# Kernel tuning notes

Measured on AMD Instinct MI355X. Metric: run time of the kernel, lower is better.

The kernel has to match this reference:

```python
import jax, jax.numpy as jnp
import numpy as np

N = 50000
LEAKY_SLOPE = 0.2


def gat_layer(x, src, dst, W, a_src, a_dst, bias, concat):
    """PyG-style GATConv (eval mode, self-loops already in src/dst).
    x: [N, Fin]; W: [Fin, H*C]; a_src, a_dst: [H, C]; bias: [H*C] or [C].
    """
    H, C = a_src.shape
    h = (x @ W).reshape(-1, H, C)                      # [N, H, C]
    alpha_src = jnp.einsum('nhc,hc->nh', h, a_src)      # [N, H]
    alpha_dst = jnp.einsum('nhc,hc->nh', h, a_dst)      # [N, H]
    e = jax.nn.leaky_relu(alpha_src[src] + alpha_dst[dst], LEAKY_SLOPE)  # [E, H]
    # scatter-softmax over incoming edges of each destination node
    m = jax.lax.stop_gradient(jax.ops.segment_max(e, dst, num_segments=N))
    e = jnp.exp(e - m[dst])
    denom = jax.ops.segment_sum(e, dst, num_segments=N)  # [N, H]
    alpha = e / (denom[dst] + 1e-16)                     # [E, H]
    msg = h[src] * alpha[:, :, None]                     # [E, H, C]
    out = jax.ops.segment_sum(msg, dst, num_segments=N)  # [N, H, C]
    out = out.reshape(-1, H * C) if concat else out.mean(axis=1)
    return out + bias


def setup_inputs() -> dict:
    key = jax.random.key(0)
    ks = jax.random.split(key, 10)
    Fin, Hd, Hh = 256, 64, 4
    E = 1600000
    x = jax.random.normal(ks[0], (N, Fin), dtype=jnp.float32)
    edge_index = jax.random.randint(ks[1], (2, E), 0, N, dtype=jnp.int64)
    s = 1.0 / np.sqrt(Fin)
    W1 = jax.random.normal(ks[2], (Fin, Hh * Hd), dtype=jnp.float32) * s
    att_src1 = jax.random.normal(ks[3], (Hh, Hd), dtype=jnp.float32) * (1.0 / np.sqrt(Hd))
    att_dst1 = jax.random.normal(ks[4], (Hh, Hd), dtype=jnp.float32) * (1.0 / np.sqrt(Hd))
    b1 = jnp.zeros((Hh * Hd,), dtype=jnp.float32)
    W2 = jax.random.normal(ks[5], (Hh * Hd, Hd), dtype=jnp.float32) * (1.0 / np.sqrt(Hh * Hd))
    att_src2 = jax.random.normal(ks[6], (1, Hd), dtype=jnp.float32) * (1.0 / np.sqrt(Hd))
    att_dst2 = jax.random.normal(ks[7], (1, Hd), dtype=jnp.float32) * (1.0 / np.sqrt(Hd))
    b2 = jnp.zeros((Hd,), dtype=jnp.float32)
    return {"x": x, "edge_index": edge_index, "W1": W1, "att_src1": att_src1,
            "att_dst1": att_dst1, "b1": b1, "W2": W2, "att_src2": att_src2,
            "att_dst2": att_dst2, "b2": b2}


def reference(x, edge_index, W1, att_src1, att_dst1, b1, W2, att_src2, att_dst2, b2):
    # PyG GATConv adds self-loops by default
    loop = jnp.arange(N, dtype=edge_index.dtype)
    src = jnp.concatenate([edge_index[0], loop])
    dst = jnp.concatenate([edge_index[1], loop])
    h = gat_layer(x, src, dst, W1, att_src1, att_dst1, b1, concat=True)
    h = jax.nn.elu(h)            # dropout is identity in eval mode
    out = gat_layer(h, src, dst, W2, att_src2, att_dst2, b2, concat=False)
    return out
```

## Files before the change

kernel.cpp:

```cpp
#include <hip/hip_runtime.h>


typedef __attribute__((ext_vector_type(8))) short short8;
typedef __attribute__((ext_vector_type(4))) float floatx4;
typedef __attribute__((ext_vector_type(2))) float fx2;

#define FIN 256
#define H1 4
#define CH 64
#define CAP 16384

__device__ __forceinline__ float bf2f(ushort u) {
    union { unsigned int i; float f; } v; v.i = ((unsigned int)u) << 16; return v.f;
}
__device__ __forceinline__ ushort f2bf(float f) {
    union { float f; unsigned int i; } v; v.f = f;
    unsigned int r = v.i + 0x7fffu + ((v.i >> 16) & 1u);
    return (ushort)(r >> 16);
}
__device__ __forceinline__ float load_in(const void* p, int i, int f) {
    return f ? ((const float*)p)[i] : bf2f(((const ushort*)p)[i]);
}
__device__ __forceinline__ int load_idx(const void* p, long long i, int f64) {
    return f64 ? (int)((const long long*)p)[i] : ((const int*)p)[i];
}

__device__ __forceinline__ float edge_p(float s) {
    s = fmaxf(s, 0.2f * s);
    return __expf(s);
}

__device__ __forceinline__ void accum16(fx2* acc, uint4 v0, uint4 v1,
                                        float p, float& l) {
    l += p;
    fx2 pv = {p, p};
    unsigned w[8] = {v0.x, v0.y, v0.z, v0.w, v1.x, v1.y, v1.z, v1.w};
#pragma unroll
    for (int u = 0; u < 8; ++u) {
        union { unsigned i; float fl; } lo, hi;
        lo.i = w[u] << 16; hi.i = w[u] & 0xffff0000u;
        fx2 c = {lo.fl, hi.fl};
        acc[u] += pv * c;
    }
}

__device__ __forceinline__ void accum8(fx2* acc, uint4 v, float p, float& l) {
    l += p;
    fx2 pv = {p, p};
    unsigned w[4] = {v.x, v.y, v.z, v.w};
#pragma unroll
    for (int u = 0; u < 4; ++u) {
        union { unsigned i; float fl; } lo, hi;
        lo.i = w[u] << 16; hi.i = w[u] & 0xffff0000u;
        fx2 c = {lo.fl, hi.fl};
        acc[u] += pv * c;
    }
}

__global__ __launch_bounds__(256) void probe_kernel(const ushort* __restrict__ x,
                                                    const int* __restrict__ ei,
                                                    int* __restrict__ flags,
                                                    int* __restrict__ bcnt) {
    __shared__ int s_nan, s_odd;
    int t = threadIdx.x;
    bcnt[t] = 0;
    if (t == 0) { s_nan = 0; s_odd = 0; }
    __syncthreads();
    int nanc = 0, oddc = 0;
    for (int i = t; i < 16384; i += 256) {
        ushort u = x[i];
        if (((u >> 7) & 0xFF) == 0xFF) nanc++;
    }
    for (int i = t; i < 2048; i += 256)
        if (ei[2 * i + 1] != 0) oddc++;
    if (nanc) atomicAdd(&s_nan, nanc);
    if (oddc) atomicAdd(&s_odd, oddc);
    __syncthreads();
    if (t == 0) {
        flags[0] = (s_nan >= 2) ? 1 : 0;
        flags[1] = (s_odd == 0) ? 1 : 0;
    }
}

__global__ __launch_bounds__(256) void prep_bucket_kernel(
        const void* __restrict__ x, const void* __restrict__ W1,
        const void* __restrict__ W2, ushort* __restrict__ xb,
        ushort* __restrict__ Wt1, ushort* __restrict__ Wt2,
        const void* __restrict__ ei, int* __restrict__ bcnt,
        unsigned int* __restrict__ buckets,
        int E, int Etot, int Nn, const int* __restrict__ flags,
        int PB_conv, int PB_tr_end) {
    __shared__ int lcnt[256], lbase[256], lcur[256];
    int bid = blockIdx.x, t = threadIdx.x;
    int f = flags[0];
    if (bid < PB_conv) {
        int i0 = bid * 2048 + t * 8;
        if (f) {
            float4 v0 = ((const float4*)x)[i0 / 4];
            float4 v1 = ((const float4*)x)[i0 / 4 + 1];
            ushort4 o0, o1;
            o0.x = f2bf(v0.x); o0.y = f2bf(v0.y); o0.z = f2bf(v0.z); o0.w = f2bf(v0.w);
            o1.x = f2bf(v1.x); o1.y = f2bf(v1.y); o1.z = f2bf(v1.z); o1.w = f2bf(v1.w);
            *(ushort4*)(xb + i0) = o0;
            *(ushort4*)(xb + i0 + 4) = o1;
        } else {
            *(uint4*)(xb + i0) = ((const uint4*)x)[i0 / 8];
        }
        return;
    }
    if (bid < PB_tr_end) {
        int j = (bid - PB_conv) * 256 + t;
        if (j < FIN * FIN) {
            int n = j / FIN, k = j % FIN;
            Wt1[j] = f2bf(load_in(W1, k * FIN + n, f));
        } else {
            int jj = j - FIN * FIN;
            int n = jj / FIN, k = jj % FIN;
            Wt2[jj] = f2bf(load_in(W2, k * CH + n, f));
        }
        return;
    }
    lcnt[t] = 0; lcur[t] = 0;
    __syncthreads();
    int f64 = flags[1];
    int base = (bid - PB_tr_end) * 4096 + t;
    unsigned int val[16]; int bk[16]; bool ok[16];
#pragma unroll
    for (int j = 0; j < 16; ++j) {
        int e = base + j * 256;
        ok[j] = e < Etot;
        bk[j] = 0; val[j] = 0;
        if (ok[j]) {
            int s, d;
            if (e < E) {
                s = load_idx(ei, e, f64);
                d = load_idx(ei, (long long)E + e, f64);
            } else {
                s = d = e - E;
            }
            s = min(max(s, 0), Nn - 1);
            d = min(max(d, 0), Nn - 1);
            bk[j] = d >> 8;
            val[j] = ((unsigned int)s << 8) | (unsigned int)(d & 255);
            atomicAdd(&lcnt[bk[j]], 1);
        }
    }
    __syncthreads();
    if (lcnt[t] > 0) lbase[t] = atomicAdd(&bcnt[t], lcnt[t]);
    __syncthreads();
#pragma unroll
    for (int j = 0; j < 16; ++j) {
        if (ok[j]) {
            int p = lbase[bk[j]] + atomicAdd(&lcur[bk[j]], 1);
            if (p < CAP) buckets[(size_t)bk[j] * CAP + p] = val[j];
        }
    }
}

__device__ __forceinline__ void gemm_core(const ushort* __restrict__ A,
                                          const ushort* __restrict__ Bt,
                                          ushort* __restrict__ C,
                                          int M, int K, int Nc,
                                          const void* __restrict__ aS,
                                          const void* __restrict__ aD,
                                          float* __restrict__ alphaS,
                                          float* __restrict__ alphaD,
                                          int H, int f, int gx, int head,
                                          int planar) {
    int tid = threadIdx.x;
    int wave = tid >> 6, lane = tid & 63, quad = lane >> 4, l16 = lane & 15;
    int rbase = gx * 256 + wave * 64;
    int cbase = head * 64;
    floatx4 acc[4][4];
#pragma unroll
    for (int i = 0; i < 4; i++)
#pragma unroll
        for (int j = 0; j < 4; j++) acc[i][j] = (floatx4)0.f;

    for (int kb = 0; kb < K; kb += 32) {
        int k0 = kb + quad * 8;
        short8 a[4], b[4];
#pragma unroll
        for (int mt = 0; mt < 4; mt++) {
            int row = rbase + mt * 16 + l16;
            if (row >= M) row = M - 1;
            a[mt] = *reinterpret_cast<const short8*>(A + (size_t)row * K + k0);
        }
#pragma unroll
        for (int nt = 0; nt < 4; nt++) {
            int col = cbase + nt * 16 + l16;
            b[nt] = *reinterpret_cast<const short8*>(Bt + (size_t)col * K + k0);
        }
#pragma unroll
        for (int mt = 0; mt < 4; mt++)
#pragma unroll
            for (int nt = 0; nt < 4; nt++)
                acc[mt][nt] = __builtin_amdgcn_mfma_f32_16x16x32_bf16(
                    a[mt], b[nt], acc[mt][nt], 0, 0, 0);
    }
    float asv[4], adv[4];
#pragma unroll
    for (int nt = 0; nt < 4; nt++) {
        int col = cbase + nt * 16 + l16;
        asv[nt] = load_in(aS, col, f);
        adv[nt] = load_in(aD, col, f);
    }
#pragma unroll
    for (int mt = 0; mt < 4; mt++) {
#pragma unroll
        for (int r = 0; r < 4; r++) {
            int row = rbase + mt * 16 + quad * 4 + r;
            float ps = 0.f, pd = 0.f;
#pragma unroll
            for (int nt = 0; nt < 4; nt++) {
                float w = acc[mt][nt][r];
                ps += w * asv[nt];
                pd += w * adv[nt];
            }
#pragma unroll
            for (int off = 8; off > 0; off >>= 1) {
                ps += __shfl_xor(ps, off, 16);
                pd += __shfl_xor(pd, off, 16);
            }
            if (row < M) {
                if (l16 == 0) {
                    alphaS[row * H + head] = ps;
                    alphaD[row * H + head] = pd;
                }
#pragma unroll
                for (int nt = 0; nt < 4; nt++) {
                    int col = cbase + nt * 16 + l16;
                    size_t caddr = planar
                        ? ((size_t)(col >> 7) * M + row) * 128 + (col & 127)
                        : (size_t)row * Nc + col;
                    C[caddr] = f2bf(acc[mt][nt][r]);
                }
            }
        }
    }
}

__global__ __launch_bounds__(256) void gemm1_pass2_kernel(
        const ushort* __restrict__ A, const ushort* __restrict__ Bt,
        ushort* __restrict__ C, int M, int K, int Nc,
        const void* __restrict__ aS, const void* __restrict__ aD,
        float* __restrict__ alphaS, float* __restrict__ alphaD,
        const int* __restrict__ flags, int g1, int nbx,
        const int* __restrict__ bcnt, const unsigned int* __restrict__ buckets,
        int* __restrict__ offs, int* __restrict__ csr_src, int Nn) {
    __shared__ int part[256], sc[256], cur[256];
    int bid = blockIdx.x;
    int t = threadIdx.x;
    if (bid < g1) {
        gemm_core(A, Bt, C, M, K, Nc, aS, aD, alphaS, alphaD, 4, flags[0],
                  bid % nbx, bid / nbx, 1);
        return;
    }
    int b = bid - g1;
    part[t] = bcnt[t];
    __syncthreads();
#pragma unroll
    for (int off = 1; off < 256; off <<= 1) {
        int v = (t >= off) ? part[t - off] : 0;
        __syncthreads();
        part[t] += v;
        __syncthreads();
    }
    int basepos = (b == 0) ? 0 : part[b - 1];
    int nEdges = min(bcnt[b], CAP);
    sc[t] = 0;
    __syncthreads();
    const unsigned int* bk = buckets + (size_t)b * CAP;
    for (int i = t; i < nEdges; i += 256)
        atomicAdd(&sc[bk[i] & 255], 1);
    __syncthreads();
    int mycount = sc[t];
    __syncthreads();
#pragma unroll
    for (int off = 1; off < 256; off <<= 1) {
        int v = (t >= off) ? sc[t - off] : 0;
        __syncthreads();
        sc[t] += v;
        __syncthreads();
    }
    int excl = sc[t] - mycount;
    int gnode = b * 256 + t;
    if (gnode <= Nn) offs[gnode] = basepos + excl;
    cur[t] = excl;
    __syncthreads();
    for (int i = t; i < nEdges; i += 256) {
        unsigned int v = bk[i];
        int p = atomicAdd(&cur[v & 255], 1);
        csr_src[basepos + p] = (int)(v >> 8);
    }
}

__global__ __launch_bounds__(256) void gemm2_kernel(const ushort* __restrict__ A,
                                                    const ushort* __restrict__ Bt,
                                                    ushort* __restrict__ C,
                                                    int M, int K, int Nc,
                                                    const void* __restrict__ aS,
                                                    const void* __restrict__ aD,
                                                    float* __restrict__ alphaS,
                                                    float* __restrict__ alphaD,
                                                    const int* __restrict__ flags) {
    gemm_core(A, Bt, C, M, K, Nc, aS, aD, alphaS, alphaD, 1, flags[0],
              blockIdx.x, blockIdx.y, 0);
}

__global__ __launch_bounds__(256) void gat_node1_pass(
        const int* __restrict__ csr_src, const int* __restrict__ offs,
        const float* __restrict__ asrc, const float* __restrict__ adst,
        const ushort* __restrict__ h1p, const void* __restrict__ b1,
        ushort* __restrict__ hmidb, int Nn, const int* __restrict__ flags,
        int plane) {
    int f = flags[0];
    int wave = threadIdx.x >> 6, lane = threadIdx.x & 63;
    int n = blockIdx.x * 4 + wave;
    if (n >= Nn) return;
    int slot = lane >> 3, cg = lane & 7;
    int head = plane * 2 + (cg >> 2);
    float ad = adst[n * H1 + head];
    unsigned rowbase = (unsigned)(plane * Nn) * 128u + (unsigned)cg * 16u;
    int beg = offs[n], end = offs[n + 1];
    fx2 acc[8];
#pragma unroll
    for (int u = 0; u < 8; ++u) acc[u] = (fx2)0.f;
    float l = 0.f;

    int e = beg;
    while (e + 16 <= end) {
        int sa = csr_src[e + slot];
        int sb = csr_src[e + 8 + slot];
        float aa = asrc[sa * H1 + head];
        float ab = asrc[sb * H1 + head];
        const uint4* ra = (const uint4*)(h1p + rowbase + (unsigned)sa * 128u);
        const uint4* rb = (const uint4*)(h1p + rowbase + (unsigned)sb * 128u);
        uint4 va0 = ra[0], va1 = ra[1];
        uint4 vb0 = rb[0], vb1 = rb[1];
        float pa = edge_p(aa + ad);
        float pb = edge_p(ab + ad);
        accum16(acc, va0, va1, pa, l);
        accum16(acc, vb0, vb1, pb, l);
        e += 16;
    }
    if (e < end) {
        int ea = e + slot, eb = e + 8 + slot;
        bool oka = ea < end, okb = eb < end;
        int sa = csr_src[oka ? ea : beg];
        int sb = csr_src[okb ? eb : beg];
        float aa = asrc[sa * H1 + head];
        float ab = asrc[sb * H1 + head];
        const uint4* ra = (const uint4*)(h1p + rowbase + (unsigned)sa * 128u);
        const uint4* rb = (const uint4*)(h1p + rowbase + (unsigned)sb * 128u);
        uint4 va0 = ra[0], va1 = ra[1];
        uint4 vb0 = rb[0], vb1 = rb[1];
        float pa = edge_p(oka ? aa + ad : -1e30f);
        float pb = edge_p(okb ? ab + ad : -1e30f);
        accum16(acc, va0, va1, pa, l);
        accum16(acc, vb0, vb1, pb, l);
    }
#pragma unroll
    for (int off = 8; off <= 32; off <<= 1) {
#pragma unroll
        for (int u = 0; u < 8; ++u) {
            acc[u][0] += __shfl_xor(acc[u][0], off);
            acc[u][1] += __shfl_xor(acc[u][1], off);
        }
        l += __shfl_xor(l, off);
    }
    if (slot == 0) {
        float inv = 1.f / (l + 1e-16f);
        int cb = plane * 128 + cg * 16;
        unsigned ow[8];
#pragma unroll
        for (int u = 0; u < 8; ++u) {
            float o0 = acc[u][0] * inv + load_in(b1, cb + 2 * u, f);
            float o1 = acc[u][1] * inv + load_in(b1, cb + 2 * u + 1, f);
            o0 = o0 > 0.f ? o0 : __expf(o0) - 1.f;
            o1 = o1 > 0.f ? o1 : __expf(o1) - 1.f;
            ow[u] = (unsigned)f2bf(o0) | ((unsigned)f2bf(o1) << 16);
        }
        uint4 st0, st1;
        st0.x = ow[0]; st0.y = ow[1]; st0.z = ow[2]; st0.w = ow[3];
        st1.x = ow[4]; st1.y = ow[5]; st1.z = ow[6]; st1.w = ow[7];
        uint4* dst = (uint4*)(hmidb + (unsigned)n * 256u + (unsigned)cb);
        dst[0] = st0; dst[1] = st1;
    }
}

__global__ __launch_bounds__(256) void gat_node2(const int* __restrict__ csr_src,
                                                 const int* __restrict__ offs,
                                                 const float* __restrict__ asrc,
                                                 const float* __restrict__ adst,
                                                 const ushort* __restrict__ h2b,
                                                 const void* __restrict__ b2,
                                                 void* __restrict__ out, int Nn,
                                                 const int* __restrict__ flags) {
    int f = flags[0];
    int wave = threadIdx.x >> 6, lane = threadIdx.x & 63;
    int n = blockIdx.x * 4 + wave;
    if (n >= Nn) return;
    int slot = lane >> 3, cg = lane & 7;
    float ad = adst[n];
    unsigned rowoff = (unsigned)cg * 8u;
    int beg = offs[n], end = offs[n + 1];
    fx2 acc[4];
#pragma unroll
    for (int u = 0; u < 4; ++u) acc[u] = (fx2)0.f;
    float l = 0.f;

    int e = beg;
    while (e + 16 <= end) {
        int sa = csr_src[e + slot];
        int sb = csr_src[e + 8 + slot];
        float aa = asrc[sa];
        float ab = asrc[sb];
        uint4 va = *(const uint4*)(h2b + rowoff + (unsigned)sa * 64u);
        uint4 vb = *(const uint4*)(h2b + rowoff + (unsigned)sb * 64u);
        float pa = edge_p(aa + ad);
        float pb = edge_p(ab + ad);
        accum8(acc, va, pa, l);
        accum8(acc, vb, pb, l);
        e += 16;
    }
    if (e < end) {
        int ea = e + slot, eb = e + 8 + slot;
        bool oka = ea < end, okb = eb < end;
        int sa = csr_src[oka ? ea : beg];
        int sb = csr_src[okb ? eb : beg];
        float aa = asrc[sa];
        float ab = asrc[sb];
        uint4 va = *(const uint4*)(h2b + rowoff + (unsigned)sa * 64u);
        uint4 vb = *(const uint4*)(h2b + rowoff + (unsigned)sb * 64u);
        float pa = edge_p(oka ? aa + ad : -1e30f);
        float pb = edge_p(okb ? ab + ad : -1e30f);
        accum8(acc, va, pa, l);
        accum8(acc, vb, pb, l);
    }
#pragma unroll
    for (int off = 8; off <= 32; off <<= 1) {
#pragma unroll
        for (int u = 0; u < 4; ++u) {
            acc[u][0] += __shfl_xor(acc[u][0], off);
            acc[u][1] += __shfl_xor(acc[u][1], off);
        }
        l += __shfl_xor(l, off);
    }
    if (slot == 0) {
        float inv = 1.f / (l + 1e-16f);
        float o[8];
#pragma unroll
        for (int u = 0; u < 4; ++u) {
            o[2 * u]     = acc[u][0] * inv + load_in(b2, cg * 8 + 2 * u, f);
            o[2 * u + 1] = acc[u][1] * inv + load_in(b2, cg * 8 + 2 * u + 1, f);
        }
        if (f) {
            float* op = (float*)out + (unsigned)n * 64u + (unsigned)cg * 8u;
            float4 s0, s1;
            s0.x = o[0]; s0.y = o[1]; s0.z = o[2]; s0.w = o[3];
            s1.x = o[4]; s1.y = o[5]; s1.z = o[6]; s1.w = o[7];
            *(float4*)op = s0;
            *(float4*)(op + 4) = s1;
        } else {
            uint4 st;
            st.x = (unsigned)f2bf(o[0]) | ((unsigned)f2bf(o[1]) << 16);
            st.y = (unsigned)f2bf(o[2]) | ((unsigned)f2bf(o[3]) << 16);
            st.z = (unsigned)f2bf(o[4]) | ((unsigned)f2bf(o[5]) << 16);
            st.w = (unsigned)f2bf(o[6]) | ((unsigned)f2bf(o[7]) << 16);
            *(uint4*)((ushort*)out + (unsigned)n * 64u + (unsigned)cg * 8u) = st;
        }
    }
}

extern "C" void kernel_launch(void* const* d_in, const int* in_sizes, int n_in,
                              void* d_out, int out_size, void* d_ws, size_t ws_size,
                              hipStream_t stream) {
    const void* x   = d_in[0];
    const void* ei  = d_in[1];
    const void* W1  = d_in[2];
    const void* as1 = d_in[3];
    const void* ad1 = d_in[4];
    const void* b1  = d_in[5];
    const void* W2  = d_in[6];
    const void* as2 = d_in[7];
    const void* ad2 = d_in[8];
    const void* b2  = d_in[9];

    const int Nn = in_sizes[0] / FIN;
    const int E  = in_sizes[1] / 2;
    const int ET = E + Nn;
    const int NB = (Nn + 255) >> 8;

    char* ws = (char*)d_ws;
    size_t off = 0;
    auto alloc = [&](size_t bytes) {
        size_t o = off;
        off += (bytes + 255) & ~(size_t)255;
        return o;
    };
    ushort* xb    = (ushort*)(ws + alloc((size_t)Nn * FIN * 2));
    ushort* h1b   = (ushort*)(ws + alloc((size_t)Nn * FIN * 2));
    ushort* hmidb = (ushort*)(ws + alloc((size_t)Nn * FIN * 2));
    ushort* h2b   = (ushort*)(ws + alloc((size_t)Nn * CH * 2));
    ushort* Wt1   = (ushort*)(ws + alloc((size_t)FIN * FIN * 2));
    ushort* Wt2   = (ushort*)(ws + alloc((size_t)CH * FIN * 2));
    float* as1f   = (float*)(ws + alloc((size_t)Nn * H1 * 4));
    float* ad1f   = (float*)(ws + alloc((size_t)Nn * H1 * 4));
    float* as2f   = (float*)(ws + alloc((size_t)Nn * 4));
    float* ad2f   = (float*)(ws + alloc((size_t)Nn * 4));
    int*   offs   = (int*)(ws + alloc((size_t)(Nn + 1) * 4));
    int*   csr    = (int*)(ws + alloc((size_t)ET * 4));
    unsigned int* buckets = (unsigned int*)(ws + alloc((size_t)256 * CAP * 4));
    int*   bcnt   = (int*)(ws + alloc(256 * 4));
    int*   flags  = (int*)(ws + alloc(256));
    (void)ws_size; (void)n_in; (void)out_size;

    probe_kernel<<<1, 256, 0, stream>>>((const ushort*)x, (const int*)ei, flags, bcnt);

    int PB_conv = (Nn * FIN) / 2048;
    int PB_tr   = (FIN * FIN + CH * FIN) / 256;
    int PB_bkt  = (ET + 4095) / 4096;
    prep_bucket_kernel<<<PB_conv + PB_tr + PB_bkt, 256, 0, stream>>>(
        x, W1, W2, xb, Wt1, Wt2, ei, bcnt, buckets,
        E, ET, Nn, flags, PB_conv, PB_conv + PB_tr);

    int nbx = (Nn + 255) / 256;
    int g1 = nbx * H1;
    gemm1_pass2_kernel<<<g1 + NB, 256, 0, stream>>>(
        xb, Wt1, h1b, Nn, FIN, FIN, as1, ad1, as1f, ad1f,
        flags, g1, nbx, bcnt, buckets, offs, csr, Nn);

    gat_node1_pass<<<(Nn + 3) / 4, 256, 0, stream>>>(
        csr, offs, as1f, ad1f, h1b, b1, hmidb, Nn, flags, 0);
    gat_node1_pass<<<(Nn + 3) / 4, 256, 0, stream>>>(
        csr, offs, as1f, ad1f, h1b, b1, hmidb, Nn, flags, 1);

    gemm2_kernel<<<dim3((Nn + 255) / 256, 1), 256, 0, stream>>>(
        hmidb, Wt2, h2b, Nn, FIN, CH, as2, ad2, as2f, ad2f, flags);
    gat_node2<<<(Nn + 3) / 4, 256, 0, stream>>>(csr, offs, as2f, ad2f, h2b, b2, d_out, Nn, flags);
}
```

Baseline: 361.6 us.

## Precompute edge softmax weights and aggregate over narrow 32-column feature planes

Adds a separate kernel that computes the per-edge exponentiated attention weights and per-node inverse denominators once and writes them to workspace. The GEMMs now write features into 32-column planes, including GEMM2, which was row-major before. The aggregation is split into 8 passes for layer 1 and 2 for layer 2, each gathering 64-byte rows. The aim is to keep each plane's gather working set cache-resident and cut per-pass work. The cost is extra launches, storing and re-reading the per-edge weight arrays, and re-reading the CSR once per pass.

```diff
diff --git a/kernel.cpp b/kernel.cpp
--- a/kernel.cpp
+++ b/kernel.cpp
@@ -30,31 +30,15 @@
     return __expf(s);
 }
 
-__device__ __forceinline__ void accum16(fx2* acc, uint4 v0, uint4 v1,
-                                        float p, float& l) {
-    l += p;
+__device__ __forceinline__ void accum4(fx2& a0, fx2& a1, uint2 v, float p) {
     fx2 pv = {p, p};
-    unsigned w[8] = {v0.x, v0.y, v0.z, v0.w, v1.x, v1.y, v1.z, v1.w};
-#pragma unroll
-    for (int u = 0; u < 8; ++u) {
-        union { unsigned i; float fl; } lo, hi;
-        lo.i = w[u] << 16; hi.i = w[u] & 0xffff0000u;
-        fx2 c = {lo.fl, hi.fl};
-        acc[u] += pv * c;
-    }
-}
-
-__device__ __forceinline__ void accum8(fx2* acc, uint4 v, float p, float& l) {
-    l += p;
-    fx2 pv = {p, p};
-    unsigned w[4] = {v.x, v.y, v.z, v.w};
-#pragma unroll
-    for (int u = 0; u < 4; ++u) {
-        union { unsigned i; float fl; } lo, hi;
-        lo.i = w[u] << 16; hi.i = w[u] & 0xffff0000u;
-        fx2 c = {lo.fl, hi.fl};
-        acc[u] += pv * c;
-    }
+    union { unsigned i; float fl; } lo, hi;
+    lo.i = v.x << 16; hi.i = v.x & 0xffff0000u;
+    fx2 c0 = {lo.fl, hi.fl};
+    a0 += pv * c0;
+    lo.i = v.y << 16; hi.i = v.y & 0xffff0000u;
+    fx2 c1 = {lo.fl, hi.fl};
+    a1 += pv * c1;
 }
 
 __global__ __launch_bounds__(256) void probe_kernel(const ushort* __restrict__ x,
@@ -231,7 +215,7 @@
                 for (int nt = 0; nt < 4; nt++) {
                     int col = cbase + nt * 16 + l16;
                     size_t caddr = planar
-                        ? ((size_t)(col >> 7) * M + row) * 128 + (col & 127)
+                        ? ((size_t)(col >> 5) * M + row) * 32 + (col & 31)
                         : (size_t)row * Nc + col;
                     C[caddr] = f2bf(acc[mt][nt][r]);
                 }
@@ -305,43 +289,76 @@
                                                     float* __restrict__ alphaD,
                                                     const int* __restrict__ flags) {
     gemm_core(A, Bt, C, M, K, Nc, aS, aD, alphaS, alphaD, 1, flags[0],
-              blockIdx.x, blockIdx.y, 0);
-}
-
-__global__ __launch_bounds__(256) void gat_node1_pass(
+              blockIdx.x, blockIdx.y, 1);
+}
+
+template <int H>
+__global__ __launch_bounds__(256) void gat_edge_w(
         const int* __restrict__ csr_src, const int* __restrict__ offs,
-        const float* __restrict__ asrc, const float* __restrict__ adst,
-        const ushort* __restrict__ h1p, const void* __restrict__ b1,
+        const float* __restrict__ asf, const float* __restrict__ adf,
+        float* __restrict__ pw, float* __restrict__ linv,
+        int Nn, int ET) {
+    int wave = threadIdx.x >> 6, lane = threadIdx.x & 63;
+    int n = blockIdx.x * 4 + wave;
+    if (n >= Nn) return;
+    int beg = offs[n], end = offs[n + 1];
+    float ad[H], l[H];
+#pragma unroll
+    for (int h = 0; h < H; ++h) { ad[h] = adf[n * H + h]; l[h] = 0.f; }
+    for (int e = beg; e < end; e += 64) {
+        int pos = e + lane;
+        bool ok = pos < end;
+        int s = csr_src[ok ? pos : beg];
+        float av[H];
+        if (H == 4) {
+            float4 v = *(const float4*)(asf + s * 4);
+            av[0] = v.x; av[1 % H] = v.y; av[2 % H] = v.z; av[3 % H] = v.w;
+        } else {
+            av[0] = asf[s];
+        }
+#pragma unroll
+        for (int h = 0; h < H; ++h) {
+            float p = edge_p(ok ? av[h] + ad[h] : -1e30f);
+            l[h] += p;
+            if (ok) pw[(size_t)h * ET + pos] = p;
+        }
+    }
+#pragma unroll
+    for (int h = 0; h < H; ++h) {
+#pragma unroll
+        for (int off = 1; off <= 32; off <<= 1) l[h] += __shfl_xor(l[h], off);
+    }
+    if (lane == 0) {
+#pragma unroll
+        for (int h = 0; h < H; ++h) linv[n * H + h] = 1.f / (l[h] + 1e-16f);
+    }
+}
+
+__global__ __launch_bounds__(256) void gat_agg1(
+        const int* __restrict__ csr_src, const int* __restrict__ offs,
+        const float* __restrict__ pw, const float* __restrict__ linv,
+        const ushort* __restrict__ plane, const void* __restrict__ b1,
         ushort* __restrict__ hmidb, int Nn, const int* __restrict__ flags,
-        int plane) {
+        int q) {
     int f = flags[0];
     int wave = threadIdx.x >> 6, lane = threadIdx.x & 63;
     int n = blockIdx.x * 4 + wave;
     if (n >= Nn) return;
     int slot = lane >> 3, cg = lane & 7;
-    int head = plane * 2 + (cg >> 2);
-    float ad = adst[n * H1 + head];
-    unsigned rowbase = (unsigned)(plane * Nn) * 128u + (unsigned)cg * 16u;
     int beg = offs[n], end = offs[n + 1];
-    fx2 acc[8];
-#pragma unroll
-    for (int u = 0; u < 8; ++u) acc[u] = (fx2)0.f;
-    float l = 0.f;
+    fx2 a0 = (fx2)0.f, a1 = (fx2)0.f;
 
     int e = beg;
     while (e + 16 <= end) {
-        int sa = csr_src[e + slot];
-        int sb = csr_src[e + 8 + slot];
-        float aa = asrc[sa * H1 + head];
-        float ab = asrc[sb * H1 + head];
-        const uint4* ra = (const uint4*)(h1p + rowbase + (unsigned)sa * 128u);
-        const uint4* rb = (const uint4*)(h1p + rowbase + (unsigned)sb * 128u);
-        uint4 va0 = ra[0], va1 = ra[1];
-        uint4 vb0 = rb[0], vb1 = rb[1];
-        float pa = edge_p(aa + ad);
-        float pb = edge_p(ab + ad);
-        accum16(acc, va0, va1, pa, l);
-        accum16(acc, vb0, vb1, pb, l);
+        int pa_ = e + slot, pb_ = e + 8 + slot;
+        int sa = __builtin_nontemporal_load(csr_src + pa_);
+        int sb = __builtin_nontemporal_load(csr_src + pb_);
+        float pa = __builtin_nontemporal_load(pw + pa_);
+        float pb = __builtin_nontemporal_load(pw + pb_);
+        uint2 va = *(const uint2*)(plane + (size_t)sa * 32 + cg * 4);
+        uint2 vb = *(const uint2*)(plane + (size_t)sb * 32 + cg * 4);
+        accum4(a0, a1, va, pa);
+        accum4(a0, a1, vb, pb);
         e += 16;
     }
     if (e < end) {
@@ -349,79 +366,63 @@
         bool oka = ea < end, okb = eb < end;
         int sa = csr_src[oka ? ea : beg];
         int sb = csr_src[okb ? eb : beg];
-        float aa = asrc[sa * H1 + head];
-        float ab = asrc[sb * H1 + head];
-        const uint4* ra = (const uint4*)(h1p + rowbase + (unsigned)sa * 128u);
-        const uint4* rb = (const uint4*)(h1p + rowbase + (unsigned)sb * 128u);
-        uint4 va0 = ra[0], va1 = ra[1];
-        uint4 vb0 = rb[0], vb1 = rb[1];
-        float pa = edge_p(oka ? aa + ad : -1e30f);
-        float pb = edge_p(okb ? ab + ad : -1e30f);
-        accum16(acc, va0, va1, pa, l);
-        accum16(acc, vb0, vb1, pb, l);
+        float pa = oka ? pw[ea] : 0.f;
+        float pb = okb ? pw[eb] : 0.f;
+        uint2 va = *(const uint2*)(plane + (size_t)sa * 32 + cg * 4);
+        uint2 vb = *(const uint2*)(plane + (size_t)sb * 32 + cg * 4);
+        accum4(a0, a1, va, pa);
+        accum4(a0, a1, vb, pb);
     }
 #pragma unroll
     for (int off = 8; off <= 32; off <<= 1) {
-#pragma unroll
-        for (int u = 0; u < 8; ++u) {
-            acc[u][0] += __shfl_xor(acc[u][0], off);
-            acc[u][1] += __shfl_xor(acc[u][1], off);
-        }
-        l += __shfl_xor(l, off);
+        a0[0] += __shfl_xor(a0[0], off);
+        a0[1] += __shfl_xor(a0[1], off);
+        a1[0] += __shfl_xor(a1[0], off);
+        a1[1] += __shfl_xor(a1[1], off);
     }
     if (slot == 0) {
-        float inv = 1.f / (l + 1e-16f);
-        int cb = plane * 128 + cg * 16;
-        unsigned ow[8];
-#pragma unroll
-        for (int u = 0; u < 8; ++u) {
-            float o0 = acc[u][0] * inv + load_in(b1, cb + 2 * u, f);
-            float o1 = acc[u][1] * inv + load_in(b1, cb + 2 * u + 1, f);
-            o0 = o0 > 0.f ? o0 : __expf(o0) - 1.f;
-            o1 = o1 > 0.f ? o1 : __expf(o1) - 1.f;
-            ow[u] = (unsigned)f2bf(o0) | ((unsigned)f2bf(o1) << 16);
-        }
-        uint4 st0, st1;
-        st0.x = ow[0]; st0.y = ow[1]; st0.z = ow[2]; st0.w = ow[3];
-        st1.x = ow[4]; st1.y = ow[5]; st1.z = ow[6]; st1.w = ow[7];
-        uint4* dst = (uint4*)(hmidb + (unsigned)n * 256u + (unsigned)cb);
-        dst[0] = st0; dst[1] = st1;
-    }
-}
-
-__global__ __launch_bounds__(256) void gat_node2(const int* __restrict__ csr_src,
-                                                 const int* __restrict__ offs,
-                                                 const float* __restrict__ asrc,
-                                                 const float* __restrict__ adst,
-                                                 const ushort* __restrict__ h2b,
-                                                 const void* __restrict__ b2,
-                                                 void* __restrict__ out, int Nn,
-                                                 const int* __restrict__ flags) {
+        float inv = linv[n * H1 + (q >> 1)];
+        int cb = q * 32 + cg * 4;
+        float o0 = a0[0] * inv + load_in(b1, cb + 0, f);
+        float o1 = a0[1] * inv + load_in(b1, cb + 1, f);
+        float o2 = a1[0] * inv + load_in(b1, cb + 2, f);
+        float o3 = a1[1] * inv + load_in(b1, cb + 3, f);
+        o0 = o0 > 0.f ? o0 : __expf(o0) - 1.f;
+        o1 = o1 > 0.f ? o1 : __expf(o1) - 1.f;
+        o2 = o2 > 0.f ? o2 : __expf(o2) - 1.f;
+        o3 = o3 > 0.f ? o3 : __expf(o3) - 1.f;
+        uint2 st;
+        st.x = (unsigned)f2bf(o0) | ((unsigned)f2bf(o1) << 16);
+        st.y = (unsigned)f2bf(o2) | ((unsigned)f2bf(o3) << 16);
+        *(uint2*)(hmidb + (size_t)n * 256 + cb) = st;
+    }
+}
+
+__global__ __launch_bounds__(256) void gat_agg2(
+        const int* __restrict__ csr_src, const int* __restrict__ offs,
+        const float* __restrict__ pw, const float* __restrict__ linv,
+        const ushort* __restrict__ plane, const void* __restrict__ b2,
+        void* __restrict__ out, int Nn, const int* __restrict__ flags,
+        int q) {
     int f = flags[0];
     int wave = threadIdx.x >> 6, lane = threadIdx.x & 63;
     int n = blockIdx.x * 4 + wave;
     if (n >= Nn) return;
     int slot = lane >> 3, cg = lane & 7;
-    float ad = adst[n];
-    unsigned rowoff = (unsigned)cg * 8u;
     int beg = offs[n], end = offs[n + 1];
-    fx2 acc[4];
-#pragma unroll
-    for (int u = 0; u < 4; ++u) acc[u] = (fx2)0.f;
-    float l = 0.f;
+    fx2 a0 = (fx2)0.f, a1 = (fx2)0.f;
 
     int e = beg;
     while (e + 16 <= end) {
-        int sa = csr_src[e + slot];
-        int sb = csr_src[e + 8 + slot];
-        float aa = asrc[sa];
-        float ab = asrc[sb];
-        uint4 va = *(const uint4*)(h2b + rowoff + (unsigned)sa * 64u);
-        uint4 vb = *(const uint4*)(h2b + rowoff + (unsigned)sb * 64u);
-        float pa = edge_p(aa + ad);
-        float pb = edge_p(ab + ad);
-        accum8(acc, va, pa, l);
-        accum8(acc, vb, pb, l);
+        int pa_ = e + slot, pb_ = e + 8 + slot;
+        int sa = __builtin_nontemporal_load(csr_src + pa_);
+        int sb = __builtin_nontemporal_load(csr_src + pb_);
+        float pa = __builtin_nontemporal_load(pw + pa_);
+        float pb = __builtin_nontemporal_load(pw + pb_);
+        uint2 va = *(const uint2*)(plane + (size_t)sa * 32 + cg * 4);
+        uint2 vb = *(const uint2*)(plane + (size_t)sb * 32 + cg * 4);
+        accum4(a0, a1, va, pa);
+        accum4(a0, a1, vb, pb);
         e += 16;
     }
     if (e < end) {
@@ -429,46 +430,35 @@
         bool oka = ea < end, okb = eb < end;
         int sa = csr_src[oka ? ea : beg];
         int sb = csr_src[okb ? eb : beg];
-        float aa = asrc[sa];
-        float ab = asrc[sb];
-        uint4 va = *(const uint4*)(h2b + rowoff + (unsigned)sa * 64u);
-        uint4 vb = *(const uint4*)(h2b + rowoff + (unsigned)sb * 64u);
-        float pa = edge_p(oka ? aa + ad : -1e30f);
-        float pb = edge_p(okb ? ab + ad : -1e30f);
-        accum8(acc, va, pa, l);
-        accum8(acc, vb, pb, l);
+        float pa = oka ? pw[ea] : 0.f;
+        float pb = okb ? pw[eb] : 0.f;
+        uint2 va = *(const uint2*)(plane + (size_t)sa * 32 + cg * 4);
+        uint2 vb = *(const uint2*)(plane + (size_t)sb * 32 + cg * 4);
+        accum4(a0, a1, va, pa);
+        accum4(a0, a1, vb, pb);
     }
 #pragma unroll
     for (int off = 8; off <= 32; off <<= 1) {
-#pragma unroll
-        for (int u = 0; u < 4; ++u) {
-            acc[u][0] += __shfl_xor(acc[u][0], off);
-            acc[u][1] += __shfl_xor(acc[u][1], off);
-        }
-        l += __shfl_xor(l, off);
+        a0[0] += __shfl_xor(a0[0], off);
+        a0[1] += __shfl_xor(a0[1], off);
+        a1[0] += __shfl_xor(a1[0], off);
+        a1[1] += __shfl_xor(a1[1], off);
     }
     if (slot == 0) {
-        float inv = 1.f / (l + 1e-16f);
-        float o[8];
-#pragma unroll
-        for (int u = 0; u < 4; ++u) {
-            o[2 * u]     = acc[u][0] * inv + load_in(b2, cg * 8 + 2 * u, f);
-            o[2 * u + 1] = acc[u][1] * inv + load_in(b2, cg * 8 + 2 * u + 1, f);
-        }
+        float inv = linv[n];
+        int cb = q * 32 + cg * 4;
+        float o0 = a0[0] * inv + load_in(b2, cb + 0, f);
+        float o1 = a0[1] * inv + load_in(b2, cb + 1, f);
+        float o2 = a1[0] * inv + load_in(b2, cb + 2, f);
+        float o3 = a1[1] * inv + load_in(b2, cb + 3, f);
         if (f) {
-            float* op = (float*)out + (unsigned)n * 64u + (unsigned)cg * 8u;
-            float4 s0, s1;
-            s0.x = o[0]; s0.y = o[1]; s0.z = o[2]; s0.w = o[3];
-            s1.x = o[4]; s1.y = o[5]; s1.z = o[6]; s1.w = o[7];
-            *(float4*)op = s0;
-            *(float4*)(op + 4) = s1;
+            float4 st; st.x = o0; st.y = o1; st.z = o2; st.w = o3;
+            *(float4*)((float*)out + (size_t)n * 64 + cb) = st;
         } else {
-            uint4 st;
-            st.x = (unsigned)f2bf(o[0]) | ((unsigned)f2bf(o[1]) << 16);
-            st.y = (unsigned)f2bf(o[2]) | ((unsigned)f2bf(o[3]) << 16);
-            st.z = (unsigned)f2bf(o[4]) | ((unsigned)f2bf(o[5]) << 16);
-            st.w = (unsigned)f2bf(o[6]) | ((unsigned)f2bf(o[7]) << 16);
-            *(uint4*)((ushort*)out + (unsigned)n * 64u + (unsigned)cg * 8u) = st;
+            uint2 st;
+            st.x = (unsigned)f2bf(o0) | ((unsigned)f2bf(o1) << 16);
+            st.y = (unsigned)f2bf(o2) | ((unsigned)f2bf(o3) << 16);
+            *(uint2*)((ushort*)out + (size_t)n * 64 + cb) = st;
         }
     }
 }
@@ -512,9 +502,15 @@
     int*   offs   = (int*)(ws + alloc((size_t)(Nn + 1) * 4));
     int*   csr    = (int*)(ws + alloc((size_t)ET * 4));
     unsigned int* buckets = (unsigned int*)(ws + alloc((size_t)256 * CAP * 4));
+    float* pw1    = (float*)(ws + alloc((size_t)H1 * ET * 4));
+    float* pw2    = (float*)(ws + alloc((size_t)ET * 4));
+    float* linv1  = (float*)(ws + alloc((size_t)Nn * H1 * 4));
+    float* linv2  = (float*)(ws + alloc((size_t)Nn * 4));
     int*   bcnt   = (int*)(ws + alloc(256 * 4));
     int*   flags  = (int*)(ws + alloc(256));
     (void)ws_size; (void)n_in; (void)out_size;
+
+    const int NBLK = (Nn + 3) / 4;
 
     probe_kernel<<<1, 256, 0, stream>>>((const ushort*)x, (const int*)ei, flags, bcnt);
 
@@ -531,12 +527,19 @@
         xb, Wt1, h1b, Nn, FIN, FIN, as1, ad1, as1f, ad1f,
         flags, g1, nbx, bcnt, buckets, offs, csr, Nn);
 
-    gat_node1_pass<<<(Nn + 3) / 4, 256, 0, stream>>>(
-        csr, offs, as1f, ad1f, h1b, b1, hmidb, Nn, flags, 0);
-    gat_node1_pass<<<(Nn + 3) / 4, 256, 0, stream>>>(
-        csr, offs, as1f, ad1f, h1b, b1, hmidb, Nn, flags, 1);
+    gat_edge_w<H1><<<NBLK, 256, 0, stream>>>(csr, offs, as1f, ad1f, pw1, linv1, Nn, ET);
+
+    for (int q = 0; q < 8; ++q) {
+        gat_agg1<<<NBLK, 256, 0, stream>>>(
+            csr, offs, pw1 + (size_t)(q >> 1) * ET, linv1,
+            h1b + (size_t)q * Nn * 32, b1, hmidb, Nn, flags, q);
+    }
 
     gemm2_kernel<<<dim3((Nn + 255) / 256, 1), 256, 0, stream>>>(
         hmidb, Wt2, h2b, Nn, FIN, CH, as2, ad2, as2f, ad2f, flags);
-    gat_node2<<<(Nn + 3) / 4, 256, 0, stream>>>(csr, offs, as2f, ad2f, h2b, b2, d_out, Nn, flags);
-}
+    gat_edge_w<1><<<NBLK, 256, 0, stream>>>(csr, offs, as2f, ad2f, pw2, linv2, Nn, ET);
+    for (int q = 0; q < 2; ++q) {
+        gat_agg2<<<NBLK, 256, 0, stream>>>(
+            csr, offs, pw2, linv2, h2b + (size_t)q * Nn * 32, b2, d_out, Nn, flags, q);
+    }
+}
```

Result: slower. 568.5 us (+57.2%).

## Pre-pack GEMM operands into MFMA fragment-tiled layout for contiguous wave loads

Applied to the files above, without the earlier changes.

The bf16 activation buffers (xb, hmidb) and the transposed weights are now written in a 16-row by 32-k tiled layout that matches the 16x16x32 MFMA fragment order. Each wave's A/B fragment load therefore becomes one contiguous 1 KB read instead of 16 rows strided by K. The K loop is fixed to FIN and unrolled by two. The row clamp is removed, so tail tiles past M read beyond the valid rows of the packed buffer. The producers (prep conversion and the node1 epilogue) now write scattered 16-byte chunks, which may cost some store efficiency.

```diff
diff --git a/kernel.cpp b/kernel.cpp
--- a/kernel.cpp
+++ b/kernel.cpp
@@ -23,6 +23,11 @@
 }
 __device__ __forceinline__ int load_idx(const void* p, long long i, int f64) {
     return f64 ? (int)((const long long*)p)[i] : ((const int*)p)[i];
+}
+
+__device__ __forceinline__ int pk_off(int row, int k, int KT) {
+    return (((row >> 4) * KT + (k >> 5)) << 9) + (((k >> 3) & 3) << 7) +
+           ((row & 15) << 3) + (k & 7);
 }
 
 __device__ __forceinline__ float edge_p(float s) {
@@ -95,16 +100,18 @@
     int f = flags[0];
     if (bid < PB_conv) {
         int i0 = bid * 2048 + t * 8;
+        int row = i0 >> 8, k = i0 & 255;
+        int po = pk_off(row, k, FIN >> 5);
         if (f) {
             float4 v0 = ((const float4*)x)[i0 / 4];
             float4 v1 = ((const float4*)x)[i0 / 4 + 1];
             ushort4 o0, o1;
             o0.x = f2bf(v0.x); o0.y = f2bf(v0.y); o0.z = f2bf(v0.z); o0.w = f2bf(v0.w);
             o1.x = f2bf(v1.x); o1.y = f2bf(v1.y); o1.z = f2bf(v1.z); o1.w = f2bf(v1.w);
-            *(ushort4*)(xb + i0) = o0;
-            *(ushort4*)(xb + i0 + 4) = o1;
+            *(ushort4*)(xb + po) = o0;
+            *(ushort4*)(xb + po + 4) = o1;
         } else {
-            *(uint4*)(xb + i0) = ((const uint4*)x)[i0 / 8];
+            *(uint4*)(xb + po) = ((const uint4*)x)[i0 / 8];
         }
         return;
     }
@@ -112,11 +119,11 @@
         int j = (bid - PB_conv) * 256 + t;
         if (j < FIN * FIN) {
             int n = j / FIN, k = j % FIN;
-            Wt1[j] = f2bf(load_in(W1, k * FIN + n, f));
+            Wt1[pk_off(n, k, FIN >> 5)] = f2bf(load_in(W1, k * FIN + n, f));
         } else {
             int jj = j - FIN * FIN;
             int n = jj / FIN, k = jj % FIN;
-            Wt2[jj] = f2bf(load_in(W2, k * CH + n, f));
+            Wt2[pk_off(n, k, FIN >> 5)] = f2bf(load_in(W2, k * CH + n, f));
         }
         return;
     }
@@ -160,36 +167,40 @@
 __device__ __forceinline__ void gemm_core(const ushort* __restrict__ A,
                                           const ushort* __restrict__ Bt,
                                           ushort* __restrict__ C,
-                                          int M, int K, int Nc,
+                                          int M, int Nc,
                                           const void* __restrict__ aS,
                                           const void* __restrict__ aD,
                                           float* __restrict__ alphaS,
                                           float* __restrict__ alphaD,
                                           int H, int f, int gx, int head,
                                           int planar) {
+    const int KT = FIN >> 5;
     int tid = threadIdx.x;
     int wave = tid >> 6, lane = tid & 63, quad = lane >> 4, l16 = lane & 15;
     int rbase = gx * 256 + wave * 64;
     int cbase = head * 64;
+    int lsub = (quad << 7) + (l16 << 3);
     floatx4 acc[4][4];
 #pragma unroll
     for (int i = 0; i < 4; i++)
 #pragma unroll
         for (int j = 0; j < 4; j++) acc[i][j] = (floatx4)0.f;
 
-    for (int kb = 0; kb < K; kb += 32) {
-        int k0 = kb + quad * 8;
+#pragma unroll 2
+    for (int kb = 0; kb < FIN; kb += 32) {
+        int kt = kb >> 5;
         short8 a[4], b[4];
 #pragma unroll
         for (int mt = 0; mt < 4; mt++) {
-            int row = rbase + mt * 16 + l16;
-            if (row >= M) row = M - 1;
-            a[mt] = *reinterpret_cast<const short8*>(A + (size_t)row * K + k0);
+            int tr = (rbase + mt * 16) >> 4;
+            a[mt] = *reinterpret_cast<const short8*>(
+                A + (((size_t)(tr * KT + kt)) << 9) + lsub);
         }
 #pragma unroll
         for (int nt = 0; nt < 4; nt++) {
-            int col = cbase + nt * 16 + l16;
-            b[nt] = *reinterpret_cast<const short8*>(Bt + (size_t)col * K + k0);
+            int tc = (cbase + nt * 16) >> 4;
+            b[nt] = *reinterpret_cast<const short8*>(
+                Bt + (((size_t)(tc * KT + kt)) << 9) + lsub);
         }
 #pragma unroll
         for (int mt = 0; mt < 4; mt++)
@@ -242,7 +253,7 @@
 
 __global__ __launch_bounds__(256) void gemm1_pass2_kernel(
         const ushort* __restrict__ A, const ushort* __restrict__ Bt,
-        ushort* __restrict__ C, int M, int K, int Nc,
+        ushort* __restrict__ C, int M, int Nc,
         const void* __restrict__ aS, const void* __restrict__ aD,
         float* __restrict__ alphaS, float* __restrict__ alphaD,
         const int* __restrict__ flags, int g1, int nbx,
@@ -252,7 +263,7 @@
     int bid = blockIdx.x;
     int t = threadIdx.x;
     if (bid < g1) {
-        gemm_core(A, Bt, C, M, K, Nc, aS, aD, alphaS, alphaD, 4, flags[0],
+        gemm_core(A, Bt, C, M, Nc, aS, aD, alphaS, alphaD, 4, flags[0],
                   bid % nbx, bid / nbx, 1);
         return;
     }
@@ -298,13 +309,13 @@
 __global__ __launch_bounds__(256) void gemm2_kernel(const ushort* __restrict__ A,
                                                     const ushort* __restrict__ Bt,
                                                     ushort* __restrict__ C,
-                                                    int M, int K, int Nc,
+                                                    int M, int Nc,
                                                     const void* __restrict__ aS,
                                                     const void* __restrict__ aD,
                                                     float* __restrict__ alphaS,
                                                     float* __restrict__ alphaD,
                                                     const int* __restrict__ flags) {
-    gemm_core(A, Bt, C, M, K, Nc, aS, aD, alphaS, alphaD, 1, flags[0],
+    gemm_core(A, Bt, C, M, Nc, aS, aD, alphaS, alphaD, 1, flags[0],
               blockIdx.x, blockIdx.y, 0);
 }
 
@@ -384,8 +395,10 @@
         uint4 st0, st1;
         st0.x = ow[0]; st0.y = ow[1]; st0.z = ow[2]; st0.w = ow[3];
         st1.x = ow[4]; st1.y = ow[5]; st1.z = ow[6]; st1.w = ow[7];
-        uint4* dst = (uint4*)(hmidb + (unsigned)n * 256u + (unsigned)cb);
-        dst[0] = st0; dst[1] = st1;
+        int po0 = pk_off(n, cb, FIN >> 5);
+        int po1 = pk_off(n, cb + 8, FIN >> 5);
+        *(uint4*)(hmidb + po0) = st0;
+        *(uint4*)(hmidb + po1) = st1;
     }
 }
 
@@ -528,7 +541,7 @@
     int nbx = (Nn + 255) / 256;
     int g1 = nbx * H1;
     gemm1_pass2_kernel<<<g1 + NB, 256, 0, stream>>>(
-        xb, Wt1, h1b, Nn, FIN, FIN, as1, ad1, as1f, ad1f,
+        xb, Wt1, h1b, Nn, FIN, as1, ad1, as1f, ad1f,
         flags, g1, nbx, bcnt, buckets, offs, csr, Nn);
 
     gat_node1_pass<<<(Nn + 3) / 4, 256, 0, stream>>>(
@@ -537,6 +550,6 @@
         csr, offs, as1f, ad1f, h1b, b1, hmidb, Nn, flags, 1);
 
     gemm2_kernel<<<dim3((Nn + 255) / 256, 1), 256, 0, stream>>>(
-        hmidb, Wt2, h2b, Nn, FIN, CH, as2, ad2, as2f, ad2f, flags);
+        hmidb, Wt2, h2b, Nn, CH, as2, ad2, as2f, ad2f, flags);
     gat_node2<<<(Nn + 3) / 4, 256, 0, stream>>>(csr, offs, as2f, ad2f, h2b, b2, d_out, Nn, flags);
 }
```

Result: no change. 366.1 us (+1.2%).
